# Optimization experiments

Hardware: AMD Instinct MI355X
Metric: run time of the kernel (lower is better)

Reference implementation:

```python
import jax, jax.numpy as jnp
import numpy as np

B, A, S, IN, H, OUT, T = 32768, 10, 50, 6, 64, 2, 60


def _p(key, shape, scale=0.1):
    return (jax.random.normal(key, shape) * scale).astype(jnp.float32)


def setup_inputs() -> dict:
    key = jax.random.key(0)
    ks = jax.random.split(key, 20)
    inp = {
        'history': jax.random.normal(ks[0], (B, A, S, IN), dtype=jnp.float32),
        # encoder layer 0 (IN->H) and layer 1 (H->H); PyTorch gate order i,f,g,o
        'enc_Wih0': _p(ks[1], (4 * H, IN)), 'enc_Whh0': _p(ks[2], (4 * H, H)),
        'enc_bih0': _p(ks[3], (4 * H,)),    'enc_bhh0': _p(ks[4], (4 * H,)),
        'enc_Wih1': _p(ks[5], (4 * H, H)),  'enc_Whh1': _p(ks[6], (4 * H, H)),
        'enc_bih1': _p(ks[7], (4 * H,)),    'enc_bhh1': _p(ks[8], (4 * H,)),
        # decoder layer 0 (OUT->H) and layer 1 (H->H)
        'dec_Wih0': _p(ks[9], (4 * H, OUT)), 'dec_Whh0': _p(ks[10], (4 * H, H)),
        'dec_bih0': _p(ks[11], (4 * H,)),    'dec_bhh0': _p(ks[12], (4 * H,)),
        'dec_Wih1': _p(ks[13], (4 * H, H)),  'dec_Whh1': _p(ks[14], (4 * H, H)),
        'dec_bih1': _p(ks[15], (4 * H,)),    'dec_bhh1': _p(ks[16], (4 * H,)),
        'lin_W': _p(ks[17], (OUT, H)), 'lin_b': _p(ks[18], (OUT,)),
        'start_token': _p(ks[19], (1, 1, OUT)),
    }
    return inp


def _cell(x, h, c, Wih, Whh, bih, bhh):
    g = x @ Wih.T + h @ Whh.T + (bih + bhh)
    i, f, gg, o = jnp.split(g, 4, axis=-1)
    c2 = jax.nn.sigmoid(f) * c + jax.nn.sigmoid(i) * jnp.tanh(gg)
    h2 = jax.nn.sigmoid(o) * jnp.tanh(c2)
    return h2, c2


def reference(history, enc_Wih0, enc_Whh0, enc_bih0, enc_bhh0,
              enc_Wih1, enc_Whh1, enc_bih1, enc_bhh1,
              dec_Wih0, dec_Whh0, dec_bih0, dec_bhh0,
              dec_Wih1, dec_Whh1, dec_bih1, dec_bhh1,
              lin_W, lin_b, start_token):
    ego = history[:, 0]                     # [B, S, IN]
    b = ego.shape[0]
    z = jnp.zeros((b, H), dtype=ego.dtype)

    def enc_step(carry, xt):
        h0, c0, h1, c1 = carry
        h0, c0 = _cell(xt, h0, c0, enc_Wih0, enc_Whh0, enc_bih0, enc_bhh0)
        h1, c1 = _cell(h0, h1, c1, enc_Wih1, enc_Whh1, enc_bih1, enc_bhh1)
        return (h0, c0, h1, c1), None

    (h0, c0, h1, c1), _ = jax.lax.scan(enc_step, (z, z, z, z),
                                       jnp.swapaxes(ego, 0, 1))  # time-major [S,B,IN]

    start = jnp.broadcast_to(start_token[0], (b, start_token.shape[2]))  # [B, OUT]

    def dec_step(carry, _):
        h0, c0, h1, c1, inp = carry
        h0, c0 = _cell(inp, h0, c0, dec_Wih0, dec_Whh0, dec_bih0, dec_bhh0)
        h1, c1 = _cell(h0, h1, c1, dec_Wih1, dec_Whh1, dec_bih1, dec_bhh1)
        out = h1 @ lin_W.T + lin_b           # [B, OUT]
        return (h0, c0, h1, c1, out), out

    _, preds = jax.lax.scan(dec_step, (h0, c0, h1, c1, start), None, length=T)
    return jnp.swapaxes(preds, 0, 1)         # [B, T, OUT]
```

## Files before the change

### kernel.cpp

```cpp
#include <hip/hip_runtime.h>
#include <stdint.h>

typedef float f32x4 __attribute__((ext_vector_type(4)));
typedef __bf16 bf16x8 __attribute__((ext_vector_type(8)));
typedef __bf16 bf16x4 __attribute__((ext_vector_type(4)));

#define SEQ 50
#define TDEC 60

static __device__ __forceinline__ float ex2(float x){return __builtin_amdgcn_exp2f(x);}
static __device__ __forceinline__ float frcp_(float x){return __builtin_amdgcn_rcpf(x);}
static __device__ __forceinline__ __bf16 bfc(float x){return (__bf16)x;}

__global__ __launch_bounds__(256,3) void lstm_s2s(
    const float* __restrict__ hist,
    const float* __restrict__ eWih0, const float* __restrict__ eWhh0,
    const float* __restrict__ ebih0, const float* __restrict__ ebhh0,
    const float* __restrict__ eWih1, const float* __restrict__ eWhh1,
    const float* __restrict__ ebih1, const float* __restrict__ ebhh1,
    const float* __restrict__ dWih0, const float* __restrict__ dWhh0,
    const float* __restrict__ dbih0, const float* __restrict__ dbhh0,
    const float* __restrict__ dWih1, const float* __restrict__ dWhh1,
    const float* __restrict__ dbih1, const float* __restrict__ dbhh1,
    const float* __restrict__ linW, const float* __restrict__ linb,
    const float* __restrict__ stok,
    float* __restrict__ out)
{
  __shared__ __bf16 xch[SEQ*16*8];
  __shared__ __bf16 hb0[2][1024];
  __shared__ __bf16 hb1[2][1024];
  __shared__ __bf16 wx0s[4*4*17*8];
  __shared__ __bf16 bf1s[4*4*17*8];
  __shared__ __bf16 wlc[2*3*4*8];
  __shared__ __bf16 obuf[16*8];

  const int tid = threadIdx.x;
  const int lane = tid & 63;
  const int w = tid >> 6;
  const int c = lane & 15;
  const int q = lane >> 4;
  const int rsel = (q == 0) ? c : 16;
  const long rowbase = (long)blockIdx.x * 16;
  const float* eg = hist + rowbase * 3000;

  union { f32x4 f; bf16x8 h; } Z;
  Z.f[0]=0.f; Z.f[1]=0.f; Z.f[2]=0.f; Z.f[3]=0.f;
  const f32x4 zero4 = Z.f;
  const bf16x8 zfrag = Z.h;
  bf16x8 onef = zfrag;
  if (q == 0) onef[0] = (__bf16)1.0f;

  const float GS[4] = {-1.442695041f,-1.442695041f,2.885390082f,-1.442695041f};

  for (int i = tid; i < 16*300; i += 256) {
    int row = i / 300, o = i - row*300;
    int t = o / 6, k = o - t*6;
    xch[(t*16+row)*8 + k] = bfc(eg[row*3000 + o]);
  }
  for (int i = tid; i < 16*SEQ; i += 256) {
    xch[i*8+6] = (__bf16)1.0f;
    xch[i*8+7] = (__bf16)0.0f;
  }
  for (int i = tid; i < 512; i += 256) {
    ((uint32_t*)hb0[0])[i] = 0u;
    ((uint32_t*)hb1[0])[i] = 0u;
  }

  auto stageWx0 = [&](const float* W, int Kin, const float* bi, const float* bh) {
    for (int i = tid; i < 272; i += 256) {
      int w2 = i / 68, rem = i - w2*68;
      int g = rem / 17, row = rem - g*17;
      __bf16* dst = wx0s + i*8;
      if (row < 16) {
        int gate = (g*4 + w2)*16 + row;
        float gs = (g==2) ? 2.885390082f : -1.442695041f;
        for (int j = 0; j < 8; ++j) {
          float v = 0.f;
          if (j < Kin) v = W[gate*Kin + j];
          else if (j == 6) v = bi[gate] + bh[gate];
          dst[j] = bfc(gs*v);
        }
      } else {
        for (int j = 0; j < 8; ++j) dst[j] = (__bf16)0.f;
      }
    }
  };
  auto stageBf1 = [&](const float* bi, const float* bh) {
    for (int i = tid; i < 272; i += 256) {
      int w2 = i / 68, rem = i - w2*68;
      int g = rem / 17, row = rem - g*17;
      __bf16* dst = bf1s + i*8;
      float v = 0.f;
      if (row < 16) {
        int gate = (g*4 + w2)*16 + row;
        float gs = (g==2) ? 2.885390082f : -1.442695041f;
        v = gs*(bi[gate] + bh[gate]);
      }
      dst[0] = bfc(v);
      for (int j = 1; j < 8; ++j) dst[j] = (__bf16)0.f;
    }
  };

  bf16x8 whL0[4][2], wxL1[4][2], whL1[4][2];
  auto loadFull = [&](const float* W, bf16x8 (*dst)[2]) {
#pragma unroll
    for (int g = 0; g < 4; ++g)
#pragma unroll
      for (int kc = 0; kc < 2; ++kc) {
        const float* p = W + ((g*4 + w)*16 + c)*64 + kc*32 + q*8;
        f32x4 a = *(const f32x4*)p;
        f32x4 b = *(const f32x4*)(p + 4);
        bf16x8 f;
        f[0]=bfc(GS[g]*a[0]); f[1]=bfc(GS[g]*a[1]);
        f[2]=bfc(GS[g]*a[2]); f[3]=bfc(GS[g]*a[3]);
        f[4]=bfc(GS[g]*b[0]); f[5]=bfc(GS[g]*b[1]);
        f[6]=bfc(GS[g]*b[2]); f[7]=bfc(GS[g]*b[3]);
        dst[g][kc] = f;
      }
  };

  const int wconst = (w>>1)*512 + (((w&1)<<1) | (q>>1))*128 + c*8 + (q&1)*4;

  float cs0[4], cs1[4];
#pragma unroll
  for (int i = 0; i < 4; ++i) { cs0[i] = 0.f; cs1[i] = 0.f; }

  auto epilogue = [&](f32x4* a, float* cs, __bf16* hnxt) {
    bf16x4 hv;
#pragma unroll
    for (int r = 0; r < 4; ++r) {
      float eI = ex2(a[0][r]);
      float eF = ex2(a[1][r]);
      float eG = ex2(a[2][r]);
      float eO = ex2(a[3][r]);
      float P  = (1.f+eI)*(eG+1.f);
      float tt = 1.f+eF;
      float D  = frcp_(tt*P);
      float c2 = (cs[r]*P + (eG-1.f)*tt)*D;
      float eC = ex2(2.885390082f*c2);
      float h2 = (eC-1.f)*frcp_((1.f+eO)*(eC+1.f));
      cs[r] = c2;
      hv[r] = bfc(h2);
    }
    *(bf16x4*)(hnxt + wconst) = hv;
    __syncthreads();
  };

  auto cellP = [&](const __bf16* xsrc, const __bf16* hcur, __bf16* hnxt, float* cs) {
    bf16x8 xf = zfrag;
    if (q == 0) xf = *(const bf16x8*)(xsrc + c*8);
    bf16x8 hf0 = *(const bf16x8*)(hcur + lane*8);
    bf16x8 hf1 = *(const bf16x8*)(hcur + 512 + lane*8);
    f32x4 a[4];
#pragma unroll
    for (int g = 0; g < 4; ++g) {
      bf16x8 wxf = *(const bf16x8*)(wx0s + ((w*4+g)*17 + rsel)*8);
      a[g] = __builtin_amdgcn_mfma_f32_16x16x32_bf16(wxf, xf, zero4, 0,0,0);
    }
#pragma unroll
    for (int g = 0; g < 4; ++g)
      a[g] = __builtin_amdgcn_mfma_f32_16x16x32_bf16(whL0[g][0], hf0, a[g], 0,0,0);
#pragma unroll
    for (int g = 0; g < 4; ++g)
      a[g] = __builtin_amdgcn_mfma_f32_16x16x32_bf16(whL0[g][1], hf1, a[g], 0,0,0);
    epilogue(a, cs, hnxt);
  };

  auto cellF = [&](const __bf16* xcur, const __bf16* hcur, __bf16* hnxt, float* cs) {
    bf16x8 xf0 = *(const bf16x8*)(xcur + lane*8);
    bf16x8 xf1 = *(const bf16x8*)(xcur + 512 + lane*8);
    bf16x8 hf0 = *(const bf16x8*)(hcur + lane*8);
    bf16x8 hf1 = *(const bf16x8*)(hcur + 512 + lane*8);
    f32x4 a[4];
#pragma unroll
    for (int g = 0; g < 4; ++g) {
      bf16x8 bfr = *(const bf16x8*)(bf1s + ((w*4+g)*17 + rsel)*8);
      a[g] = __builtin_amdgcn_mfma_f32_16x16x32_bf16(bfr, onef, zero4, 0,0,0);
    }
#pragma unroll
    for (int g = 0; g < 4; ++g)
      a[g] = __builtin_amdgcn_mfma_f32_16x16x32_bf16(wxL1[g][0], xf0, a[g], 0,0,0);
#pragma unroll
    for (int g = 0; g < 4; ++g)
      a[g] = __builtin_amdgcn_mfma_f32_16x16x32_bf16(wxL1[g][1], xf1, a[g], 0,0,0);
#pragma unroll
    for (int g = 0; g < 4; ++g)
      a[g] = __builtin_amdgcn_mfma_f32_16x16x32_bf16(whL1[g][0], hf0, a[g], 0,0,0);
#pragma unroll
    for (int g = 0; g < 4; ++g)
      a[g] = __builtin_amdgcn_mfma_f32_16x16x32_bf16(whL1[g][1], hf1, a[g], 0,0,0);
    epilogue(a, cs, hnxt);
  };

  stageWx0(eWih0, 6, ebih0, ebhh0);
  stageBf1(ebih1, ebhh1);
  loadFull(eWhh0, whL0);
  loadFull(eWih1, wxL1);
  loadFull(eWhh1, whL1);
  __syncthreads();

  int pc = 0;
#pragma unroll 1
  for (int t = 0; t < SEQ; ++t) {
    cellP(xch + t*128, hb0[pc], hb0[pc^1], cs0);
    cellF(hb0[pc^1], hb1[pc], hb1[pc^1], cs1);
    pc ^= 1;
  }

  stageWx0(dWih0, 2, dbih0, dbhh0);
  stageBf1(dbih1, dbhh1);
  loadFull(dWhh0, whL0);
  loadFull(dWih1, wxL1);
  loadFull(dWhh1, whL1);
  for (int i = tid; i < 24; i += 256) {
    int kc = i / 12, rem = i - kc*12;
    int row = rem / 4, q2 = rem - row*4;
    __bf16* dst = wlc + i*8;
    for (int j = 0; j < 8; ++j)
      dst[j] = (row < 2) ? bfc(linW[row*64 + kc*32 + q2*8 + j]) : (__bf16)0.f;
  }
  {
    float s0 = stok[0], s1 = stok[1];
    for (int i = tid; i < 16; i += 256) {
      obuf[i*8+0] = bfc(s0);
      obuf[i*8+1] = bfc(s1);
      obuf[i*8+2] = (__bf16)0.f;
      obuf[i*8+3] = (__bf16)0.f;
      obuf[i*8+4] = (__bf16)0.f;
      obuf[i*8+5] = (__bf16)0.f;
      obuf[i*8+6] = (__bf16)1.0f;
      obuf[i*8+7] = (__bf16)0.f;
    }
  }
  const float lb0 = linb[0], lb1 = linb[1];
  __syncthreads();

#pragma unroll 1
  for (int t = 0; t < TDEC; ++t) {
    cellP(obuf, hb0[pc], hb0[pc^1], cs0);
    cellF(hb0[pc^1], hb1[pc], hb1[pc^1], cs1);
    if (w == 0) {
      const __bf16* h1 = hb1[pc^1];
      bf16x8 xf0 = *(const bf16x8*)(h1 + lane*8);
      bf16x8 xf1 = *(const bf16x8*)(h1 + 512 + lane*8);
      int hr = (c < 2) ? c : 2;
      bf16x8 wl0 = *(const bf16x8*)(wlc + hr*32 + q*8);
      bf16x8 wl1 = *(const bf16x8*)(wlc + 96 + hr*32 + q*8);
      f32x4 oa = __builtin_amdgcn_mfma_f32_16x16x32_bf16(wl0, xf0, zero4, 0,0,0);
      oa = __builtin_amdgcn_mfma_f32_16x16x32_bf16(wl1, xf1, oa, 0,0,0);
      if (q == 0) {
        float v0 = oa[0] + lb0, v1 = oa[1] + lb1;
        float2 vv; vv.x = v0; vv.y = v1;
        *(float2*)(out + (rowbase + c)*120 + t*2) = vv;
        obuf[c*8+0] = bfc(v0);
        obuf[c*8+1] = bfc(v1);
      }
    }
    __syncthreads();
    pc ^= 1;
  }
}

extern "C" void kernel_launch(void* const* d_in, const int* in_sizes, int n_in,
                              void* d_out, int out_size, void* d_ws, size_t ws_size,
                              hipStream_t stream) {
  (void)in_sizes; (void)n_in; (void)d_ws; (void)ws_size; (void)out_size;
  const float* p[20];
  for (int i = 0; i < 20; ++i) p[i] = (const float*)d_in[i];
  dim3 grid(2048), block(256);
  hipLaunchKernelGGL(lstm_s2s, grid, block, 0, stream,
                     p[0], p[1], p[2], p[3], p[4], p[5], p[6], p[7], p[8], p[9],
                     p[10], p[11], p[12], p[13], p[14], p[15], p[16], p[17], p[18], p[19],
                     (float*)d_out);
}
```

Before: 1.047 ms.

## Software-pipeline LSTM layers and compute decoder projection redundantly per wave

Restructures each timestep so layer-1's recurrent matmul (on the previous h1) is issued before layer-0's epilogue, and layer-0's next-step recurrent matmul is computed right after the new h0 is available, so matrix work overlaps the transcendental epilogues. Layer-1 bias is now added as the MFMA accumulator init instead of through an extra bias MFMA. Every wave now computes the output projection itself and keeps the fed-back input in registers, which removes the obuf round trip and one barrier. Outputs are buffered in LDS and written out with coalesced vector stores at the end. The cost is more register pressure and redundant projection MFMAs in every wave.

```diff
diff --git a/kernel.cpp b/kernel.cpp
--- a/kernel.cpp
+++ b/kernel.cpp
@@ -2,6 +2,7 @@
 #include <stdint.h>
 
 typedef float f32x4 __attribute__((ext_vector_type(4)));
+typedef float f32x2 __attribute__((ext_vector_type(2)));
 typedef __bf16 bf16x8 __attribute__((ext_vector_type(8)));
 typedef __bf16 bf16x4 __attribute__((ext_vector_type(4)));
 
@@ -30,9 +31,9 @@
   __shared__ __bf16 hb0[2][1024];
   __shared__ __bf16 hb1[2][1024];
   __shared__ __bf16 wx0s[4*4*17*8];
-  __shared__ __bf16 bf1s[4*4*17*8];
+  __shared__ float  bC1[256];
   __shared__ __bf16 wlc[2*3*4*8];
-  __shared__ __bf16 obuf[16*8];
+  __shared__ float  obf[16*124];
 
   const int tid = threadIdx.x;
   const int lane = tid & 63;
@@ -47,8 +48,6 @@
   Z.f[0]=0.f; Z.f[1]=0.f; Z.f[2]=0.f; Z.f[3]=0.f;
   const f32x4 zero4 = Z.f;
   const bf16x8 zfrag = Z.h;
-  bf16x8 onef = zfrag;
-  if (q == 0) onef[0] = (__bf16)1.0f;
 
   const float GS[4] = {-1.442695041f,-1.442695041f,2.885390082f,-1.442695041f};
 
@@ -85,19 +84,12 @@
       }
     }
   };
-  auto stageBf1 = [&](const float* bi, const float* bh) {
-    for (int i = tid; i < 272; i += 256) {
-      int w2 = i / 68, rem = i - w2*68;
-      int g = rem / 17, row = rem - g*17;
-      __bf16* dst = bf1s + i*8;
-      float v = 0.f;
-      if (row < 16) {
-        int gate = (g*4 + w2)*16 + row;
-        float gs = (g==2) ? 2.885390082f : -1.442695041f;
-        v = gs*(bi[gate] + bh[gate]);
-      }
-      dst[0] = bfc(v);
-      for (int j = 1; j < 8; ++j) dst[j] = (__bf16)0.f;
+  auto stageBc1 = [&](const float* bi, const float* bh) {
+    for (int i = tid; i < 256; i += 256) {
+      int w2 = i >> 6, g = (i >> 4) & 3, q2 = (i >> 2) & 3, r = i & 3;
+      int gate = (g*4 + w2)*16 + q2*4 + r;
+      float gs = (g==2) ? 2.885390082f : -1.442695041f;
+      bC1[i] = gs*(bi[gate] + bh[gate]);
     }
   };
 
@@ -143,72 +135,78 @@
       hv[r] = bfc(h2);
     }
     *(bf16x4*)(hnxt + wconst) = hv;
-    __syncthreads();
   };
 
-  auto cellP = [&](const __bf16* xsrc, const __bf16* hcur, __bf16* hnxt, float* cs) {
-    bf16x8 xf = zfrag;
-    if (q == 0) xf = *(const bf16x8*)(xsrc + c*8);
-    bf16x8 hf0 = *(const bf16x8*)(hcur + lane*8);
-    bf16x8 hf1 = *(const bf16x8*)(hcur + 512 + lane*8);
-    f32x4 a[4];
-#pragma unroll
-    for (int g = 0; g < 4; ++g) {
-      bf16x8 wxf = *(const bf16x8*)(wx0s + ((w*4+g)*17 + rsel)*8);
-      a[g] = __builtin_amdgcn_mfma_f32_16x16x32_bf16(wxf, xf, zero4, 0,0,0);
-    }
-#pragma unroll
-    for (int g = 0; g < 4; ++g)
-      a[g] = __builtin_amdgcn_mfma_f32_16x16x32_bf16(whL0[g][0], hf0, a[g], 0,0,0);
-#pragma unroll
-    for (int g = 0; g < 4; ++g)
-      a[g] = __builtin_amdgcn_mfma_f32_16x16x32_bf16(whL0[g][1], hf1, a[g], 0,0,0);
-    epilogue(a, cs, hnxt);
-  };
-
-  auto cellF = [&](const __bf16* xcur, const __bf16* hcur, __bf16* hnxt, float* cs) {
-    bf16x8 xf0 = *(const bf16x8*)(xcur + lane*8);
-    bf16x8 xf1 = *(const bf16x8*)(xcur + 512 + lane*8);
-    bf16x8 hf0 = *(const bf16x8*)(hcur + lane*8);
-    bf16x8 hf1 = *(const bf16x8*)(hcur + 512 + lane*8);
-    f32x4 a[4];
-#pragma unroll
-    for (int g = 0; g < 4; ++g) {
-      bf16x8 bfr = *(const bf16x8*)(bf1s + ((w*4+g)*17 + rsel)*8);
-      a[g] = __builtin_amdgcn_mfma_f32_16x16x32_bf16(bfr, onef, zero4, 0,0,0);
-    }
-#pragma unroll
-    for (int g = 0; g < 4; ++g)
-      a[g] = __builtin_amdgcn_mfma_f32_16x16x32_bf16(wxL1[g][0], xf0, a[g], 0,0,0);
-#pragma unroll
-    for (int g = 0; g < 4; ++g)
-      a[g] = __builtin_amdgcn_mfma_f32_16x16x32_bf16(wxL1[g][1], xf1, a[g], 0,0,0);
-#pragma unroll
-    for (int g = 0; g < 4; ++g)
-      a[g] = __builtin_amdgcn_mfma_f32_16x16x32_bf16(whL1[g][0], hf0, a[g], 0,0,0);
-#pragma unroll
-    for (int g = 0; g < 4; ++g)
-      a[g] = __builtin_amdgcn_mfma_f32_16x16x32_bf16(whL1[g][1], hf1, a[g], 0,0,0);
-    epilogue(a, cs, hnxt);
-  };
-
   stageWx0(eWih0, 6, ebih0, ebhh0);
-  stageBf1(ebih1, ebhh1);
+  stageBc1(ebih1, ebhh1);
   loadFull(eWhh0, whL0);
   loadFull(eWih1, wxL1);
   loadFull(eWhh1, whL1);
   __syncthreads();
 
+  f32x4 acc0[4];
+  {
+    bf16x8 xf = zfrag;
+    if (q == 0) xf = *(const bf16x8*)(xch + c*8);
+#pragma unroll
+    for (int g = 0; g < 4; ++g) {
+      bf16x8 wxf = *(const bf16x8*)(wx0s + ((w*4+g)*17 + rsel)*8);
+      acc0[g] = __builtin_amdgcn_mfma_f32_16x16x32_bf16(wxf, xf, zero4, 0,0,0);
+    }
+  }
+
   int pc = 0;
 #pragma unroll 1
   for (int t = 0; t < SEQ; ++t) {
-    cellP(xch + t*128, hb0[pc], hb0[pc^1], cs0);
-    cellF(hb0[pc^1], hb1[pc], hb1[pc^1], cs1);
+    f32x4 acc1[4];
+    {
+      const __bf16* h1p = hb1[pc];
+      bf16x8 hf0 = *(const bf16x8*)(h1p + lane*8);
+      bf16x8 hf1 = *(const bf16x8*)(h1p + 512 + lane*8);
+#pragma unroll
+      for (int g = 0; g < 4; ++g) {
+        f32x4 bi4 = *(const f32x4*)(bC1 + w*64 + g*16 + q*4);
+        acc1[g] = __builtin_amdgcn_mfma_f32_16x16x32_bf16(whL1[g][0], hf0, bi4, 0,0,0);
+      }
+#pragma unroll
+      for (int g = 0; g < 4; ++g)
+        acc1[g] = __builtin_amdgcn_mfma_f32_16x16x32_bf16(whL1[g][1], hf1, acc1[g], 0,0,0);
+    }
+    epilogue(acc0, cs0, hb0[pc^1]);
+    __syncthreads();
+    {
+      const __bf16* h0n = hb0[pc^1];
+      bf16x8 xf0 = *(const bf16x8*)(h0n + lane*8);
+      bf16x8 xf1 = *(const bf16x8*)(h0n + 512 + lane*8);
+#pragma unroll
+      for (int g = 0; g < 4; ++g)
+        acc1[g] = __builtin_amdgcn_mfma_f32_16x16x32_bf16(wxL1[g][0], xf0, acc1[g], 0,0,0);
+#pragma unroll
+      for (int g = 0; g < 4; ++g)
+        acc1[g] = __builtin_amdgcn_mfma_f32_16x16x32_bf16(wxL1[g][1], xf1, acc1[g], 0,0,0);
+      epilogue(acc1, cs1, hb1[pc^1]);
+      if (t + 1 < SEQ) {
+        bf16x8 xf = zfrag;
+        if (q == 0) xf = *(const bf16x8*)(xch + (t+1)*128 + c*8);
+#pragma unroll
+        for (int g = 0; g < 4; ++g) {
+          bf16x8 wxf = *(const bf16x8*)(wx0s + ((w*4+g)*17 + rsel)*8);
+          acc0[g] = __builtin_amdgcn_mfma_f32_16x16x32_bf16(wxf, xf, zero4, 0,0,0);
+        }
+#pragma unroll
+        for (int g = 0; g < 4; ++g)
+          acc0[g] = __builtin_amdgcn_mfma_f32_16x16x32_bf16(whL0[g][0], xf0, acc0[g], 0,0,0);
+#pragma unroll
+        for (int g = 0; g < 4; ++g)
+          acc0[g] = __builtin_amdgcn_mfma_f32_16x16x32_bf16(whL0[g][1], xf1, acc0[g], 0,0,0);
+      }
+    }
+    __syncthreads();
     pc ^= 1;
   }
 
   stageWx0(dWih0, 2, dbih0, dbhh0);
-  stageBf1(dbih1, dbhh1);
+  stageBc1(dbih1, dbhh1);
   loadFull(dWhh0, whL0);
   loadFull(dWih1, wxL1);
   loadFull(dWhh1, whL1);
@@ -219,45 +217,102 @@
     for (int j = 0; j < 8; ++j)
       dst[j] = (row < 2) ? bfc(linW[row*64 + kc*32 + q2*8 + j]) : (__bf16)0.f;
   }
+  const float lb0 = linb[0], lb1 = linb[1];
+  const float s0 = stok[0], s1 = stok[1];
+  __syncthreads();
+
+  bf16x8 xdec = zfrag;
+  if (q == 0) { xdec[0] = bfc(s0); xdec[1] = bfc(s1); xdec[6] = (__bf16)1.0f; }
   {
-    float s0 = stok[0], s1 = stok[1];
-    for (int i = tid; i < 16; i += 256) {
-      obuf[i*8+0] = bfc(s0);
-      obuf[i*8+1] = bfc(s1);
-      obuf[i*8+2] = (__bf16)0.f;
-      obuf[i*8+3] = (__bf16)0.f;
-      obuf[i*8+4] = (__bf16)0.f;
-      obuf[i*8+5] = (__bf16)0.f;
-      obuf[i*8+6] = (__bf16)1.0f;
-      obuf[i*8+7] = (__bf16)0.f;
-    }
-  }
-  const float lb0 = linb[0], lb1 = linb[1];
-  __syncthreads();
+    const __bf16* h0p = hb0[pc];
+    bf16x8 hf0 = *(const bf16x8*)(h0p + lane*8);
+    bf16x8 hf1 = *(const bf16x8*)(h0p + 512 + lane*8);
+#pragma unroll
+    for (int g = 0; g < 4; ++g) {
+      bf16x8 wxf = *(const bf16x8*)(wx0s + ((w*4+g)*17 + rsel)*8);
+      acc0[g] = __builtin_amdgcn_mfma_f32_16x16x32_bf16(wxf, xdec, zero4, 0,0,0);
+    }
+#pragma unroll
+    for (int g = 0; g < 4; ++g)
+      acc0[g] = __builtin_amdgcn_mfma_f32_16x16x32_bf16(whL0[g][0], hf0, acc0[g], 0,0,0);
+#pragma unroll
+    for (int g = 0; g < 4; ++g)
+      acc0[g] = __builtin_amdgcn_mfma_f32_16x16x32_bf16(whL0[g][1], hf1, acc0[g], 0,0,0);
+  }
 
 #pragma unroll 1
   for (int t = 0; t < TDEC; ++t) {
-    cellP(obuf, hb0[pc], hb0[pc^1], cs0);
-    cellF(hb0[pc^1], hb1[pc], hb1[pc^1], cs1);
-    if (w == 0) {
-      const __bf16* h1 = hb1[pc^1];
-      bf16x8 xf0 = *(const bf16x8*)(h1 + lane*8);
-      bf16x8 xf1 = *(const bf16x8*)(h1 + 512 + lane*8);
+    f32x4 acc1[4];
+    {
+      const __bf16* h1p = hb1[pc];
+      bf16x8 hf0 = *(const bf16x8*)(h1p + lane*8);
+      bf16x8 hf1 = *(const bf16x8*)(h1p + 512 + lane*8);
+#pragma unroll
+      for (int g = 0; g < 4; ++g) {
+        f32x4 bi4 = *(const f32x4*)(bC1 + w*64 + g*16 + q*4);
+        acc1[g] = __builtin_amdgcn_mfma_f32_16x16x32_bf16(whL1[g][0], hf0, bi4, 0,0,0);
+      }
+#pragma unroll
+      for (int g = 0; g < 4; ++g)
+        acc1[g] = __builtin_amdgcn_mfma_f32_16x16x32_bf16(whL1[g][1], hf1, acc1[g], 0,0,0);
+    }
+    epilogue(acc0, cs0, hb0[pc^1]);
+    __syncthreads();
+    {
+      const __bf16* h0n = hb0[pc^1];
+      bf16x8 xf0 = *(const bf16x8*)(h0n + lane*8);
+      bf16x8 xf1 = *(const bf16x8*)(h0n + 512 + lane*8);
+#pragma unroll
+      for (int g = 0; g < 4; ++g)
+        acc1[g] = __builtin_amdgcn_mfma_f32_16x16x32_bf16(wxL1[g][0], xf0, acc1[g], 0,0,0);
+#pragma unroll
+      for (int g = 0; g < 4; ++g)
+        acc1[g] = __builtin_amdgcn_mfma_f32_16x16x32_bf16(wxL1[g][1], xf1, acc1[g], 0,0,0);
+      epilogue(acc1, cs1, hb1[pc^1]);
+      if (t + 1 < TDEC) {
+#pragma unroll
+        for (int g = 0; g < 4; ++g)
+          acc0[g] = __builtin_amdgcn_mfma_f32_16x16x32_bf16(whL0[g][0], xf0, zero4, 0,0,0);
+#pragma unroll
+        for (int g = 0; g < 4; ++g)
+          acc0[g] = __builtin_amdgcn_mfma_f32_16x16x32_bf16(whL0[g][1], xf1, acc0[g], 0,0,0);
+      }
+    }
+    __syncthreads();
+    {
+      const __bf16* h1n = hb1[pc^1];
+      bf16x8 xh0 = *(const bf16x8*)(h1n + lane*8);
+      bf16x8 xh1 = *(const bf16x8*)(h1n + 512 + lane*8);
       int hr = (c < 2) ? c : 2;
       bf16x8 wl0 = *(const bf16x8*)(wlc + hr*32 + q*8);
       bf16x8 wl1 = *(const bf16x8*)(wlc + 96 + hr*32 + q*8);
-      f32x4 oa = __builtin_amdgcn_mfma_f32_16x16x32_bf16(wl0, xf0, zero4, 0,0,0);
-      oa = __builtin_amdgcn_mfma_f32_16x16x32_bf16(wl1, xf1, oa, 0,0,0);
+      f32x4 oa = __builtin_amdgcn_mfma_f32_16x16x32_bf16(wl0, xh0, zero4, 0,0,0);
+      oa = __builtin_amdgcn_mfma_f32_16x16x32_bf16(wl1, xh1, oa, 0,0,0);
       if (q == 0) {
         float v0 = oa[0] + lb0, v1 = oa[1] + lb1;
-        float2 vv; vv.x = v0; vv.y = v1;
-        *(float2*)(out + (rowbase + c)*120 + t*2) = vv;
-        obuf[c*8+0] = bfc(v0);
-        obuf[c*8+1] = bfc(v1);
-      }
-    }
-    __syncthreads();
+        if (w == 0) {
+          f32x2 vv; vv[0] = v0; vv[1] = v1;
+          *(f32x2*)(obf + c*124 + t*2) = vv;
+        }
+        xdec[0] = bfc(v0); xdec[1] = bfc(v1);
+      }
+      if (t + 1 < TDEC) {
+#pragma unroll
+        for (int g = 0; g < 4; ++g) {
+          bf16x8 wxf = *(const bf16x8*)(wx0s + ((w*4+g)*17 + rsel)*8);
+          acc0[g] = __builtin_amdgcn_mfma_f32_16x16x32_bf16(wxf, xdec, acc0[g], 0,0,0);
+        }
+      }
+    }
     pc ^= 1;
+  }
+
+  __syncthreads();
+  for (int i = tid; i < 480; i += 256) {
+    int row = i / 30;
+    int j = (i - row*30) * 4;
+    f32x4 v = *(const f32x4*)(obf + row*124 + j);
+    *(f32x4*)(out + rowbase*120 + i*4) = v;
   }
 }
 
```

Result: no change. 1.055 ms (+0.7%).
